# Optimization experiments

Measured on AMD Instinct MI355X. Metric: run time of the kernel, lower is better.

The kernel has to match this reference:

```python
import jax, jax.numpy as jnp
import numpy as np

NUM_EMBEDDINGS = 1024
EMBEDDING_DIM = 64
BETA = 0.25  # commitment_cost


def setup_inputs() -> dict:
    key = jax.random.key(0)
    k1, k2 = jax.random.split(key)
    z = jax.random.normal(k1, (32, EMBEDDING_DIM, 32, 32), dtype=jnp.float32)
    embedding = jax.random.normal(k2, (NUM_EMBEDDINGS, EMBEDDING_DIM), dtype=jnp.float32)
    return {"z": z, "embedding": embedding}


def reference(z, embedding):
    B, D, H, W = z.shape
    beta = jnp.asarray(BETA, z.dtype)
    # [B, D, H, W] -> [B*H*W, D]
    z_flat = jnp.transpose(z, (0, 2, 3, 1)).reshape(-1, D)
    # squared L2 distances to each code: ||z||^2 - 2 z.e^T + ||e||^2  -> [N, E]
    dist = (
        jnp.sum(z_flat * z_flat, axis=1, keepdims=True)
        - 2.0 * (z_flat @ embedding.T)
        + jnp.sum(embedding * embedding, axis=1)
    )
    encoding_indices = jnp.argmin(dist, axis=1)  # [N]
    # direct gather instead of one-hot matmul (same math)
    quantized = embedding[encoding_indices]  # [N, D]
    quantized = jnp.transpose(quantized.reshape(B, H, W, D), (0, 3, 1, 2))
    commitment_loss = beta * jnp.mean(
        (jax.lax.stop_gradient(z) - quantized) ** 2
    )
    codebook_loss = jnp.mean((z - jax.lax.stop_gradient(quantized)) ** 2)
    loss = commitment_loss + codebook_loss
    # straight-through estimator
    quantized_st = z + jax.lax.stop_gradient(quantized - z)
    return (quantized_st, loss, encoding_indices)
```

## Files before the change

kernel.cpp:

```cpp
#include <hip/hip_runtime.h>

typedef __attribute__((ext_vector_type(8))) short short8;
typedef __attribute__((ext_vector_type(4))) float f32x4;
typedef unsigned int uint32;

#define QOUT 2097152

__device__ __forceinline__ unsigned short f2bf(float f){
  uint32 u = __float_as_uint(f);
  return (unsigned short)((u + 0x7FFFu + ((u >> 16) & 1u)) >> 16);
}
__device__ __forceinline__ float bf2f(unsigned short h){
  return __uint_as_float(((uint32)h) << 16);
}
__device__ __forceinline__ uint32 med3u(uint32 a, uint32 b, uint32 c){
  uint32 d;
  asm("v_med3_u32 %0, %1, %2, %3" : "=v"(d) : "v"(a), "v"(b), "v"(c));
  return d;
}

__global__ void vq_prep(const float* __restrict__ emb, unsigned char* __restrict__ ebg,
                        float* __restrict__ nrm64, int* __restrict__ cnt){
  int u = blockIdx.x * 256 + threadIdx.x;
  if (u == 0) *cnt = 0;
  int C = u >> 3, oct = u & 7;
  const float4* e4 = reinterpret_cast<const float4*>(emb) + C * 16 + oct * 2;
  float4 v0 = e4[0], v1 = e4[1];
  float vv[8] = {v0.x, v0.y, v0.z, v0.w, v1.x, v1.y, v1.z, v1.w};
  float s = 0.f;
  short8 H, L;
#pragma unroll
  for (int j = 0; j < 8; ++j){
    float v = vv[j];
    s = fmaf(v, v, s);
    unsigned short hs = f2bf(v);
    unsigned short ls = f2bf(v - bf2f(hs));
    H[j] = (short)hs; L[j] = (short)ls;
  }
  int ng = C >> 4, c15 = C & 15, kf = oct >> 2, gg = oct & 3;
  unsigned char* base = ebg + ng * 4096 + kf * 2048 + (gg * 16 + c15) * 16;
  *reinterpret_cast<short8*>(base) = H;
  *reinterpret_cast<short8*>(base + 1024) = L;
#pragma unroll
  for (int d = 1; d < 8; d <<= 1) s += __shfl_xor(s, d);
  if (oct == 0) nrm64[C] = 0.5f * s + 128.0f;
}

__global__ __launch_bounds__(256, 2) void vq_main(
    const float* __restrict__ z, const float* __restrict__ emb,
    const unsigned char* __restrict__ ebg, const float* __restrict__ nrm64,
    float* __restrict__ out, float* __restrict__ partial, int* __restrict__ cnt)
{
  __shared__ float zf[64 * 68];
  __shared__ float nrmlds[1024];
  __shared__ uint32 mg[64][2][3];
  __shared__ uint32 cand[64][3];
  __shared__ int kidx[64];
  __shared__ int flagrow[64];
  __shared__ int nflag;
  __shared__ float werr[4];
  __shared__ float red[256];
  __shared__ int isLast;

  const int t = threadIdx.x;
  const int bi = blockIdx.x;
  const int n0 = bi * 64;
  const int b = n0 >> 10;
  const int hw0 = n0 & 1023;
  const int w = t >> 6, lane = t & 63;
  const int wm = w >> 1, wn = w & 1;
  const int l15 = lane & 15, g = lane >> 4;

#pragma unroll
  for (int i = 0; i < 4; ++i) nrmlds[i * 256 + t] = nrm64[i * 256 + t];
  if (t == 255) nflag = 0;

#pragma unroll
  for (int k = 0; k < 16; ++k){
    int li = k * 256 + t;
    int d = li >> 6, j = li & 63;
    zf[j * 68 + d] = z[((b * 64 + d) << 10) + hw0 + j];
  }
  __syncthreads();

  short8 ah[2][2], al[2][2];
#pragma unroll
  for (int mf = 0; mf < 2; ++mf)
#pragma unroll
    for (int kf = 0; kf < 2; ++kf){
      int row = wm * 32 + mf * 16 + l15;
      int base = row * 68 + kf * 32 + g * 8;
      float4 q0 = *reinterpret_cast<float4*>(&zf[base]);
      float4 q1 = *reinterpret_cast<float4*>(&zf[base + 4]);
      float vv[8] = {q0.x,q0.y,q0.z,q0.w,q1.x,q1.y,q1.z,q1.w};
#pragma unroll
      for (int j = 0; j < 8; ++j){
        float v = -vv[j];
        unsigned short hs = f2bf(v);
        unsigned short ls = f2bf(v - bf2f(hs));
        ah[mf][kf][j] = (short)hs;
        al[mf][kf][j] = (short)ls;
      }
    }

  uint32 u0[8], u1[8], u2[8];
#pragma unroll
  for (int s = 0; s < 8; ++s){ u0[s] = 0xFFFFFFFFu; u1[s] = 0xFFFFFFFFu; u2[s] = 0xFFFFFFFFu; }

  const unsigned char* pbase = ebg + (wn << 17) + (lane << 4);
  short8 fb[3][4];

#pragma unroll
  for (int s = 0; s < 2; ++s){
    const unsigned char* p = pbase + (s << 12);
    fb[s][0] = *reinterpret_cast<const short8*>(p);
    fb[s][1] = *reinterpret_cast<const short8*>(p + 1024);
    fb[s][2] = *reinterpret_cast<const short8*>(p + 2048);
    fb[s][3] = *reinterpret_cast<const short8*>(p + 3072);
  }

#pragma unroll
  for (int i = 0; i < 32; ++i){
    if (i < 30){
      const unsigned char* p = pbase + ((i + 2) << 12);
      fb[(i + 2) % 3][0] = *reinterpret_cast<const short8*>(p);
      fb[(i + 2) % 3][1] = *reinterpret_cast<const short8*>(p + 1024);
      fb[(i + 2) % 3][2] = *reinterpret_cast<const short8*>(p + 2048);
      fb[(i + 2) % 3][3] = *reinterpret_cast<const short8*>(p + 3072);
    }
    __builtin_amdgcn_sched_barrier(0);
    short8 bh0 = fb[i % 3][0];
    short8 bl0 = fb[i % 3][1];
    short8 bh1 = fb[i % 3][2];
    short8 bl1 = fb[i % 3][3];
    int code = ((wn * 32 + i) << 4) + l15;
    float nv = nrmlds[code];
    f32x4 a0 = {nv, nv, nv, nv};
    f32x4 a1 = {nv, nv, nv, nv};
    a0 = __builtin_amdgcn_mfma_f32_16x16x32_bf16(ah[0][0], bh0, a0, 0,0,0);
    a0 = __builtin_amdgcn_mfma_f32_16x16x32_bf16(ah[0][1], bh1, a0, 0,0,0);
    a0 = __builtin_amdgcn_mfma_f32_16x16x32_bf16(al[0][0], bh0, a0, 0,0,0);
    a0 = __builtin_amdgcn_mfma_f32_16x16x32_bf16(al[0][1], bh1, a0, 0,0,0);
    a0 = __builtin_amdgcn_mfma_f32_16x16x32_bf16(ah[0][0], bl0, a0, 0,0,0);
    a0 = __builtin_amdgcn_mfma_f32_16x16x32_bf16(ah[0][1], bl1, a0, 0,0,0);
    a1 = __builtin_amdgcn_mfma_f32_16x16x32_bf16(ah[1][0], bh0, a1, 0,0,0);
    a1 = __builtin_amdgcn_mfma_f32_16x16x32_bf16(ah[1][1], bh1, a1, 0,0,0);
    a1 = __builtin_amdgcn_mfma_f32_16x16x32_bf16(al[1][0], bh0, a1, 0,0,0);
    a1 = __builtin_amdgcn_mfma_f32_16x16x32_bf16(al[1][1], bh1, a1, 0,0,0);
    a1 = __builtin_amdgcn_mfma_f32_16x16x32_bf16(ah[1][0], bl0, a1, 0,0,0);
    a1 = __builtin_amdgcn_mfma_f32_16x16x32_bf16(ah[1][1], bl1, a1, 0,0,0);
    uint32 kb = (uint32)code;
#pragma unroll
    for (int r = 0; r < 4; ++r){
      uint32 k0v = (__float_as_uint(a0[r]) & 0xFFFFFC00u) | kb;
      u2[r] = med3u(k0v, u1[r], u2[r]);
      u1[r] = med3u(k0v, u0[r], u1[r]);
      u0[r] = u0[r] < k0v ? u0[r] : k0v;
      uint32 k1v = (__float_as_uint(a1[r]) & 0xFFFFFC00u) | kb;
      u2[4+r] = med3u(k1v, u1[4+r], u2[4+r]);
      u1[4+r] = med3u(k1v, u0[4+r], u1[4+r]);
      u0[4+r] = u0[4+r] < k1v ? u0[4+r] : k1v;
    }
  }

#pragma unroll
  for (int dm = 1; dm < 16; dm <<= 1){
#pragma unroll
    for (int s = 0; s < 8; ++s){
      uint32 x0 = (uint32)__shfl_xor((int)u0[s], dm);
      uint32 x1 = (uint32)__shfl_xor((int)u1[s], dm);
      uint32 x2 = (uint32)__shfl_xor((int)u2[s], dm);
      u2[s] = med3u(x0, u1[s], u2[s]); u1[s] = med3u(x0, u0[s], u1[s]); u0[s] = u0[s] < x0 ? u0[s] : x0;
      u2[s] = med3u(x1, u1[s], u2[s]); u1[s] = med3u(x1, u0[s], u1[s]); u0[s] = u0[s] < x1 ? u0[s] : x1;
      u2[s] = med3u(x2, u1[s], u2[s]); u1[s] = med3u(x2, u0[s], u1[s]); u0[s] = u0[s] < x2 ? u0[s] : x2;
    }
  }
  if (l15 == 0){
#pragma unroll
    for (int mf = 0; mf < 2; ++mf)
#pragma unroll
      for (int r = 0; r < 4; ++r){
        int lr = wm * 32 + mf * 16 + g * 4 + r;
        int s = mf * 4 + r;
        mg[lr][wn][0] = u0[s]; mg[lr][wn][1] = u1[s]; mg[lr][wn][2] = u2[s];
      }
  }
  __syncthreads();

  if (t < 64){
    uint32 a0k = mg[t][0][0], a1k = mg[t][0][1], a2k = mg[t][0][2];
#pragma unroll
    for (int j2 = 0; j2 < 3; ++j2){
      uint32 x = mg[t][1][j2];
      a2k = med3u(x, a1k, a2k); a1k = med3u(x, a0k, a1k); a0k = a0k < x ? a0k : x;
    }
    kidx[t] = (int)(a0k & 1023u);
    cand[t][0] = a0k; cand[t][1] = a1k; cand[t][2] = a2k;
    float d0 = __uint_as_float(a0k & 0xFFFFFC00u);
    float d1 = __uint_as_float(a1k & 0xFFFFFC00u);
    if (d1 - d0 < 0.0625f){
      int pos = atomicAdd(&nflag, 1);
      flagrow[pos] = t;
    }
  }
  __syncthreads();

  {
    int nf = nflag;
    int cidx = lane >> 4, q = lane & 15;
    for (int n = w; n < nf; n += 4){
      int row = flagrow[n];
      double acc = 0.0;
      if (cidx < 3){
        int k = (int)(cand[row][cidx] & 1023u);
        float4 ev = *reinterpret_cast<const float4*>(emb + k * 64 + q * 4);
        float4 zv = *reinterpret_cast<const float4*>(&zf[row * 68 + q * 4]);
        double d0v = (double)zv.x - (double)ev.x;
        double d1v = (double)zv.y - (double)ev.y;
        double d2v = (double)zv.z - (double)ev.z;
        double d3v = (double)zv.w - (double)ev.w;
        acc = d0v*d0v + d1v*d1v + d2v*d2v + d3v*d3v;
      }
#pragma unroll
      for (int dx = 1; dx < 16; dx <<= 1) acc += __shfl_xor(acc, dx);
      double s0 = __shfl(acc, 0);
      double s1 = __shfl(acc, 16);
      double s2 = __shfl(acc, 32);
      if (lane == 0){
        int k0 = (int)(cand[row][0] & 1023u);
        int k1 = (int)(cand[row][1] & 1023u);
        int k2 = (int)(cand[row][2] & 1023u);
        int bk = k0; double bs = s0;
        if (s1 < bs || (s1 == bs && k1 < bk)) { bs = s1; bk = k1; }
        if (s2 < bs || (s2 == bs && k2 < bk)) { bs = s2; bk = k2; }
        kidx[row] = bk;
      }
    }
  }
  __syncthreads();

  {
    int row = t & 63, dp = t >> 6;
    int k = kidx[row];
    const float4* e4p = reinterpret_cast<const float4*>(emb + k * 64 + dp * 16);
    float4 ev0 = e4p[0], ev1 = e4p[1], ev2 = e4p[2], ev3 = e4p[3];
    float evf[16] = {ev0.x,ev0.y,ev0.z,ev0.w, ev1.x,ev1.y,ev1.z,ev1.w,
                     ev2.x,ev2.y,ev2.z,ev2.w, ev3.x,ev3.y,ev3.z,ev3.w};
    float* ob = out + (b << 16) + hw0 + row;
    float err = 0.f;
#pragma unroll
    for (int dd = 0; dd < 16; ++dd){
      int d = dp * 16 + dd;
      float zv = zf[row * 68 + d];
      float qv = evf[dd];
      ob[d << 10] = qv;
      float df = zv - qv;
      err = fmaf(df, df, err);
    }
    if (dp == 0) out[QOUT + 1 + n0 + row] = (float)k;
#pragma unroll
    for (int dx = 1; dx < 64; dx <<= 1) err += __shfl_xor(err, dx);
    if (lane == 0) werr[w] = err;
  }
  __syncthreads();
  if (t == 0){
    partial[bi] = (werr[0] + werr[1]) + (werr[2] + werr[3]);
    __threadfence();
    int pos = atomicAdd(cnt, 1);
    isLast = (pos == 511) ? 1 : 0;
  }
  __syncthreads();

  if (isLast){
    __threadfence();
    const volatile float* vp = partial;
    red[t] = vp[t] + vp[t + 256];
    __syncthreads();
    for (int ww = 128; ww > 0; ww >>= 1){
      if (t < ww) red[t] += red[t + ww];
      __syncthreads();
    }
    if (t == 0) out[QOUT] = 1.25f * red[0] * (1.0f / 2097152.0f);
  }
}

extern "C" void kernel_launch(void* const* d_in, const int* in_sizes, int n_in,
                              void* d_out, int out_size, void* d_ws, size_t ws_size,
                              hipStream_t stream) {
  const float* z   = (const float*)d_in[0];
  const float* emb = (const float*)d_in[1];
  float* out = (float*)d_out;
  unsigned char* ebg = (unsigned char*)d_ws;
  float* nrm64   = (float*)(ebg + 262144);
  float* partial = nrm64 + 1024;
  int*   cnt     = (int*)(partial + 512);

  vq_prep <<<32,  256, 0, stream>>>(emb, ebg, nrm64, cnt);
  vq_main <<<512, 256, 0, stream>>>(z, emb, ebg, nrm64, out, partial, cnt);
}
```

Baseline: 43.46 us.

## Split codebook scan across eight waves per block and drop manual prefetch

```diff
diff --git a/kernel.cpp b/kernel.cpp
--- a/kernel.cpp
+++ b/kernel.cpp
@@ -46,19 +46,19 @@
   if (oct == 0) nrm64[C] = 0.5f * s + 128.0f;
 }
 
-__global__ __launch_bounds__(256, 2) void vq_main(
+__global__ __launch_bounds__(512, 4) void vq_main(
     const float* __restrict__ z, const float* __restrict__ emb,
     const unsigned char* __restrict__ ebg, const float* __restrict__ nrm64,
     float* __restrict__ out, float* __restrict__ partial, int* __restrict__ cnt)
 {
   __shared__ float zf[64 * 68];
   __shared__ float nrmlds[1024];
-  __shared__ uint32 mg[64][2][3];
+  __shared__ uint32 mg[64][4][3];
   __shared__ uint32 cand[64][3];
   __shared__ int kidx[64];
   __shared__ int flagrow[64];
   __shared__ int nflag;
-  __shared__ float werr[4];
+  __shared__ float werr[8];
   __shared__ float red[256];
   __shared__ int isLast;
 
@@ -68,16 +68,16 @@
   const int b = n0 >> 10;
   const int hw0 = n0 & 1023;
   const int w = t >> 6, lane = t & 63;
-  const int wm = w >> 1, wn = w & 1;
+  const int wm = w >> 2, wn = w & 3;
   const int l15 = lane & 15, g = lane >> 4;
 
 #pragma unroll
-  for (int i = 0; i < 4; ++i) nrmlds[i * 256 + t] = nrm64[i * 256 + t];
-  if (t == 255) nflag = 0;
-
-#pragma unroll
-  for (int k = 0; k < 16; ++k){
-    int li = k * 256 + t;
+  for (int i = 0; i < 2; ++i) nrmlds[i * 512 + t] = nrm64[i * 512 + t];
+  if (t == 0) nflag = 0;
+
+#pragma unroll
+  for (int k = 0; k < 8; ++k){
+    int li = k * 512 + t;
     int d = li >> 6, j = li & 63;
     zf[j * 68 + d] = z[((b * 64 + d) << 10) + hw0 + j];
   }
@@ -107,33 +107,15 @@
 #pragma unroll
   for (int s = 0; s < 8; ++s){ u0[s] = 0xFFFFFFFFu; u1[s] = 0xFFFFFFFFu; u2[s] = 0xFFFFFFFFu; }
 
-  const unsigned char* pbase = ebg + (wn << 17) + (lane << 4);
-  short8 fb[3][4];
-
-#pragma unroll
-  for (int s = 0; s < 2; ++s){
-    const unsigned char* p = pbase + (s << 12);
-    fb[s][0] = *reinterpret_cast<const short8*>(p);
-    fb[s][1] = *reinterpret_cast<const short8*>(p + 1024);
-    fb[s][2] = *reinterpret_cast<const short8*>(p + 2048);
-    fb[s][3] = *reinterpret_cast<const short8*>(p + 3072);
-  }
-
-#pragma unroll
-  for (int i = 0; i < 32; ++i){
-    if (i < 30){
-      const unsigned char* p = pbase + ((i + 2) << 12);
-      fb[(i + 2) % 3][0] = *reinterpret_cast<const short8*>(p);
-      fb[(i + 2) % 3][1] = *reinterpret_cast<const short8*>(p + 1024);
-      fb[(i + 2) % 3][2] = *reinterpret_cast<const short8*>(p + 2048);
-      fb[(i + 2) % 3][3] = *reinterpret_cast<const short8*>(p + 3072);
-    }
-    __builtin_amdgcn_sched_barrier(0);
-    short8 bh0 = fb[i % 3][0];
-    short8 bl0 = fb[i % 3][1];
-    short8 bh1 = fb[i % 3][2];
-    short8 bl1 = fb[i % 3][3];
-    int code = ((wn * 32 + i) << 4) + l15;
+  const unsigned char* pbase = ebg + (wn << 16) + (lane << 4);
+#pragma unroll
+  for (int i = 0; i < 16; ++i){
+    const unsigned char* p = pbase + (i << 12);
+    short8 bh0 = *reinterpret_cast<const short8*>(p);
+    short8 bl0 = *reinterpret_cast<const short8*>(p + 1024);
+    short8 bh1 = *reinterpret_cast<const short8*>(p + 2048);
+    short8 bl1 = *reinterpret_cast<const short8*>(p + 3072);
+    int code = ((wn * 16 + i) << 4) + l15;
     float nv = nrmlds[code];
     f32x4 a0 = {nv, nv, nv, nv};
     f32x4 a1 = {nv, nv, nv, nv};
@@ -190,10 +172,12 @@
   if (t < 64){
     uint32 a0k = mg[t][0][0], a1k = mg[t][0][1], a2k = mg[t][0][2];
 #pragma unroll
-    for (int j2 = 0; j2 < 3; ++j2){
-      uint32 x = mg[t][1][j2];
-      a2k = med3u(x, a1k, a2k); a1k = med3u(x, a0k, a1k); a0k = a0k < x ? a0k : x;
-    }
+    for (int v = 1; v < 4; ++v)
+#pragma unroll
+      for (int j2 = 0; j2 < 3; ++j2){
+        uint32 x = mg[t][v][j2];
+        a2k = med3u(x, a1k, a2k); a1k = med3u(x, a0k, a1k); a0k = a0k < x ? a0k : x;
+      }
     kidx[t] = (int)(a0k & 1023u);
     cand[t][0] = a0k; cand[t][1] = a1k; cand[t][2] = a2k;
     float d0 = __uint_as_float(a0k & 0xFFFFFC00u);
@@ -208,7 +192,7 @@
   {
     int nf = nflag;
     int cidx = lane >> 4, q = lane & 15;
-    for (int n = w; n < nf; n += 4){
+    for (int n = w; n < nf; n += 8){
       int row = flagrow[n];
       double acc = 0.0;
       if (cidx < 3){
@@ -242,15 +226,14 @@
   {
     int row = t & 63, dp = t >> 6;
     int k = kidx[row];
-    const float4* e4p = reinterpret_cast<const float4*>(emb + k * 64 + dp * 16);
-    float4 ev0 = e4p[0], ev1 = e4p[1], ev2 = e4p[2], ev3 = e4p[3];
-    float evf[16] = {ev0.x,ev0.y,ev0.z,ev0.w, ev1.x,ev1.y,ev1.z,ev1.w,
-                     ev2.x,ev2.y,ev2.z,ev2.w, ev3.x,ev3.y,ev3.z,ev3.w};
+    const float4* e4p = reinterpret_cast<const float4*>(emb + k * 64 + dp * 8);
+    float4 ev0 = e4p[0], ev1 = e4p[1];
+    float evf[8] = {ev0.x,ev0.y,ev0.z,ev0.w, ev1.x,ev1.y,ev1.z,ev1.w};
     float* ob = out + (b << 16) + hw0 + row;
     float err = 0.f;
 #pragma unroll
-    for (int dd = 0; dd < 16; ++dd){
-      int d = dp * 16 + dd;
+    for (int dd = 0; dd < 8; ++dd){
+      int d = dp * 8 + dd;
       float zv = zf[row * 68 + d];
       float qv = evf[dd];
       ob[d << 10] = qv;
@@ -264,7 +247,8 @@
   }
   __syncthreads();
   if (t == 0){
-    partial[bi] = (werr[0] + werr[1]) + (werr[2] + werr[3]);
+    partial[bi] = ((werr[0] + werr[1]) + (werr[2] + werr[3]))
+                + ((werr[4] + werr[5]) + (werr[6] + werr[7]));
     __threadfence();
     int pos = atomicAdd(cnt, 1);
     isLast = (pos == 511) ? 1 : 0;
@@ -273,8 +257,10 @@
 
   if (isLast){
     __threadfence();
-    const volatile float* vp = partial;
-    red[t] = vp[t] + vp[t + 256];
+    if (t < 256){
+      const volatile float* vp = partial;
+      red[t] = vp[t] + vp[t + 256];
+    }
     __syncthreads();
     for (int ww = 128; ww > 0; ww >>= 1){
       if (t < ww) red[t] += red[t + ww];
@@ -296,5 +282,5 @@
   int*   cnt     = (int*)(partial + 512);
 
   vq_prep <<<32,  256, 0, stream>>>(emb, ebg, nrm64, cnt);
-  vq_main <<<512, 256, 0, stream>>>(z, emb, ebg, nrm64, out, partial, cnt);
-}
+  vq_main <<<512, 512, 0, stream>>>(z, emb, ebg, nrm64, out, partial, cnt);
+}
```

New measurement: 45.70 us. +5.2%, slower.

## Stage codebook chunks in LDS via global_load_lds with swizzled layout

Applied to the files above, without the earlier changes.

```diff
diff --git a/kernel.cpp b/kernel.cpp
--- a/kernel.cpp
+++ b/kernel.cpp
@@ -17,6 +17,11 @@
   uint32 d;
   asm("v_med3_u32 %0, %1, %2, %3" : "=v"(d) : "v"(a), "v"(b), "v"(c));
   return d;
+}
+__device__ __forceinline__ void glds16(const unsigned char* g, unsigned char* l){
+  __builtin_amdgcn_global_load_lds(
+      (const __attribute__((address_space(1))) unsigned int*)g,
+      (__attribute__((address_space(3))) unsigned int*)l, 16, 0, 0);
 }
 
 __global__ void vq_prep(const float* __restrict__ emb, unsigned char* __restrict__ ebg,
@@ -24,23 +29,25 @@
   int u = blockIdx.x * 256 + threadIdx.x;
   if (u == 0) *cnt = 0;
   int C = u >> 3, oct = u & 7;
-  const float4* e4 = reinterpret_cast<const float4*>(emb) + C * 16 + oct * 2;
-  float4 v0 = e4[0], v1 = e4[1];
-  float vv[8] = {v0.x, v0.y, v0.z, v0.w, v1.x, v1.y, v1.z, v1.w};
+  int chunk = C >> 8, cc = C & 255;
+  unsigned char* eb = ebg + chunk * 65536;
+  int x = (cc & 7) << 1;
+  const float4* e4 = reinterpret_cast<const float4*>(emb) + C * 16;
   float s = 0.f;
-  short8 H, L;
-#pragma unroll
-  for (int j = 0; j < 8; ++j){
-    float v = vv[j];
-    s = fmaf(v, v, s);
-    unsigned short hs = f2bf(v);
-    unsigned short ls = f2bf(v - bf2f(hs));
-    H[j] = (short)hs; L[j] = (short)ls;
-  }
-  int ng = C >> 4, c15 = C & 15, kf = oct >> 2, gg = oct & 3;
-  unsigned char* base = ebg + ng * 4096 + kf * 2048 + (gg * 16 + c15) * 16;
-  *reinterpret_cast<short8*>(base) = H;
-  *reinterpret_cast<short8*>(base + 1024) = L;
+#pragma unroll
+  for (int si = 0; si < 2; ++si){
+    int sub = oct * 2 + si;
+    float4 v = e4[sub];
+    s += v.x*v.x + v.y*v.y + v.z*v.z + v.w*v.w;
+    ushort4 h, l;
+    h.x = f2bf(v.x); l.x = f2bf(v.x - bf2f(h.x));
+    h.y = f2bf(v.y); l.y = f2bf(v.y - bf2f(h.y));
+    h.z = f2bf(v.z); l.z = f2bf(v.z - bf2f(h.z));
+    h.w = f2bf(v.w); l.w = f2bf(v.w - bf2f(h.w));
+    int off = cc * 128 + ((sub ^ x) << 3);
+    *reinterpret_cast<ushort4*>(eb + off) = h;
+    *reinterpret_cast<ushort4*>(eb + 32768 + off) = l;
+  }
 #pragma unroll
   for (int d = 1; d < 8; d <<= 1) s += __shfl_xor(s, d);
   if (oct == 0) nrm64[C] = 0.5f * s + 128.0f;
@@ -51,7 +58,7 @@
     const unsigned char* __restrict__ ebg, const float* __restrict__ nrm64,
     float* __restrict__ out, float* __restrict__ partial, int* __restrict__ cnt)
 {
-  __shared__ float zf[64 * 68];
+  __shared__ __align__(16) unsigned char LB[65536];
   __shared__ float nrmlds[1024];
   __shared__ uint32 mg[64][2][3];
   __shared__ uint32 cand[64][3];
@@ -71,10 +78,10 @@
   const int wm = w >> 1, wn = w & 1;
   const int l15 = lane & 15, g = lane >> 4;
 
-#pragma unroll
-  for (int i = 0; i < 4; ++i) nrmlds[i * 256 + t] = nrm64[i * 256 + t];
-  if (t == 255) nflag = 0;
-
+  for (int i = t; i < 1024; i += 256) nrmlds[i] = nrm64[i];
+  if (t == 0) nflag = 0;
+
+  float* zf = reinterpret_cast<float*>(LB);
 #pragma unroll
   for (int k = 0; k < 16; ++k){
     int li = k * 256 + t;
@@ -102,65 +109,63 @@
         al[mf][kf][j] = (short)ls;
       }
     }
+  __syncthreads();
 
   uint32 u0[8], u1[8], u2[8];
 #pragma unroll
   for (int s = 0; s < 8; ++s){ u0[s] = 0xFFFFFFFFu; u1[s] = 0xFFFFFFFFu; u2[s] = 0xFFFFFFFFu; }
 
-  const unsigned char* pbase = ebg + (wn << 17) + (lane << 4);
-  short8 fb[3][4];
-
-#pragma unroll
-  for (int s = 0; s < 2; ++s){
-    const unsigned char* p = pbase + (s << 12);
-    fb[s][0] = *reinterpret_cast<const short8*>(p);
-    fb[s][1] = *reinterpret_cast<const short8*>(p + 1024);
-    fb[s][2] = *reinterpret_cast<const short8*>(p + 2048);
-    fb[s][3] = *reinterpret_cast<const short8*>(p + 3072);
-  }
-
-#pragma unroll
-  for (int i = 0; i < 32; ++i){
-    if (i < 30){
-      const unsigned char* p = pbase + ((i + 2) << 12);
-      fb[(i + 2) % 3][0] = *reinterpret_cast<const short8*>(p);
-      fb[(i + 2) % 3][1] = *reinterpret_cast<const short8*>(p + 1024);
-      fb[(i + 2) % 3][2] = *reinterpret_cast<const short8*>(p + 2048);
-      fb[(i + 2) % 3][3] = *reinterpret_cast<const short8*>(p + 3072);
-    }
-    __builtin_amdgcn_sched_barrier(0);
-    short8 bh0 = fb[i % 3][0];
-    short8 bl0 = fb[i % 3][1];
-    short8 bh1 = fb[i % 3][2];
-    short8 bl1 = fb[i % 3][3];
-    int code = ((wn * 32 + i) << 4) + l15;
-    float nv = nrmlds[code];
-    f32x4 a0 = {nv, nv, nv, nv};
-    f32x4 a1 = {nv, nv, nv, nv};
-    a0 = __builtin_amdgcn_mfma_f32_16x16x32_bf16(ah[0][0], bh0, a0, 0,0,0);
-    a0 = __builtin_amdgcn_mfma_f32_16x16x32_bf16(ah[0][1], bh1, a0, 0,0,0);
-    a0 = __builtin_amdgcn_mfma_f32_16x16x32_bf16(al[0][0], bh0, a0, 0,0,0);
-    a0 = __builtin_amdgcn_mfma_f32_16x16x32_bf16(al[0][1], bh1, a0, 0,0,0);
-    a0 = __builtin_amdgcn_mfma_f32_16x16x32_bf16(ah[0][0], bl0, a0, 0,0,0);
-    a0 = __builtin_amdgcn_mfma_f32_16x16x32_bf16(ah[0][1], bl1, a0, 0,0,0);
-    a1 = __builtin_amdgcn_mfma_f32_16x16x32_bf16(ah[1][0], bh0, a1, 0,0,0);
-    a1 = __builtin_amdgcn_mfma_f32_16x16x32_bf16(ah[1][1], bh1, a1, 0,0,0);
-    a1 = __builtin_amdgcn_mfma_f32_16x16x32_bf16(al[1][0], bh0, a1, 0,0,0);
-    a1 = __builtin_amdgcn_mfma_f32_16x16x32_bf16(al[1][1], bh1, a1, 0,0,0);
-    a1 = __builtin_amdgcn_mfma_f32_16x16x32_bf16(ah[1][0], bl0, a1, 0,0,0);
-    a1 = __builtin_amdgcn_mfma_f32_16x16x32_bf16(ah[1][1], bl1, a1, 0,0,0);
-    uint32 kb = (uint32)code;
-#pragma unroll
-    for (int r = 0; r < 4; ++r){
-      uint32 k0v = (__float_as_uint(a0[r]) & 0xFFFFFC00u) | kb;
-      u2[r] = med3u(k0v, u1[r], u2[r]);
-      u1[r] = med3u(k0v, u0[r], u1[r]);
-      u0[r] = u0[r] < k0v ? u0[r] : k0v;
-      uint32 k1v = (__float_as_uint(a1[r]) & 0xFFFFFC00u) | kb;
-      u2[4+r] = med3u(k1v, u1[4+r], u2[4+r]);
-      u1[4+r] = med3u(k1v, u0[4+r], u1[4+r]);
-      u0[4+r] = u0[4+r] < k1v ? u0[4+r] : k1v;
-    }
+  const int cc0 = wn * 128 + l15;
+  const int xsw = (l15 & 7) << 1;
+  const int v0s = ((g * 2) ^ xsw) << 3;
+  const int v1s = ((8 + g * 2) ^ xsw) << 3;
+
+  for (int c = 0; c < 4; ++c){
+    const unsigned char* src = ebg + c * 65536;
+#pragma unroll
+    for (int r = 0; r < 16; ++r){
+      int off = (r * 4 + w) * 1024;
+      glds16(src + off + lane * 16, LB + off);
+    }
+    __syncthreads();
+
+#pragma unroll
+    for (int nf = 0; nf < 8; ++nf){
+      int cc = cc0 + nf * 16;
+      const unsigned char* rb = LB + cc * 128;
+      short8 bh0 = *reinterpret_cast<const short8*>(rb + v0s);
+      short8 bh1 = *reinterpret_cast<const short8*>(rb + v1s);
+      short8 bl0 = *reinterpret_cast<const short8*>(rb + 32768 + v0s);
+      short8 bl1 = *reinterpret_cast<const short8*>(rb + 32768 + v1s);
+      float nv = nrmlds[(c << 8) + cc];
+      f32x4 a0 = {nv, nv, nv, nv};
+      f32x4 a1 = {nv, nv, nv, nv};
+      a0 = __builtin_amdgcn_mfma_f32_16x16x32_bf16(ah[0][0], bh0, a0, 0,0,0);
+      a0 = __builtin_amdgcn_mfma_f32_16x16x32_bf16(ah[0][1], bh1, a0, 0,0,0);
+      a0 = __builtin_amdgcn_mfma_f32_16x16x32_bf16(al[0][0], bh0, a0, 0,0,0);
+      a0 = __builtin_amdgcn_mfma_f32_16x16x32_bf16(al[0][1], bh1, a0, 0,0,0);
+      a0 = __builtin_amdgcn_mfma_f32_16x16x32_bf16(ah[0][0], bl0, a0, 0,0,0);
+      a0 = __builtin_amdgcn_mfma_f32_16x16x32_bf16(ah[0][1], bl1, a0, 0,0,0);
+      a1 = __builtin_amdgcn_mfma_f32_16x16x32_bf16(ah[1][0], bh0, a1, 0,0,0);
+      a1 = __builtin_amdgcn_mfma_f32_16x16x32_bf16(ah[1][1], bh1, a1, 0,0,0);
+      a1 = __builtin_amdgcn_mfma_f32_16x16x32_bf16(al[1][0], bh0, a1, 0,0,0);
+      a1 = __builtin_amdgcn_mfma_f32_16x16x32_bf16(al[1][1], bh1, a1, 0,0,0);
+      a1 = __builtin_amdgcn_mfma_f32_16x16x32_bf16(ah[1][0], bl0, a1, 0,0,0);
+      a1 = __builtin_amdgcn_mfma_f32_16x16x32_bf16(ah[1][1], bl1, a1, 0,0,0);
+      uint32 kb = (uint32)((c << 8) | cc0 | (nf << 4));
+#pragma unroll
+      for (int r = 0; r < 4; ++r){
+        uint32 k0v = (__float_as_uint(a0[r]) & 0xFFFFFC00u) | kb;
+        u2[r] = med3u(k0v, u1[r], u2[r]);
+        u1[r] = med3u(k0v, u0[r], u1[r]);
+        u0[r] = u0[r] < k0v ? u0[r] : k0v;
+        uint32 k1v = (__float_as_uint(a1[r]) & 0xFFFFFC00u) | kb;
+        u2[4+r] = med3u(k1v, u1[4+r], u2[4+r]);
+        u1[4+r] = med3u(k1v, u0[4+r], u1[4+r]);
+        u0[4+r] = u0[4+r] < k1v ? u0[4+r] : k1v;
+      }
+    }
+    __syncthreads();
   }
 
 #pragma unroll
@@ -207,18 +212,18 @@
 
   {
     int nf = nflag;
-    int cidx = lane >> 4, q = lane & 15;
+    int cidx = lane >> 4, qd = lane & 15;
     for (int n = w; n < nf; n += 4){
       int row = flagrow[n];
       double acc = 0.0;
       if (cidx < 3){
         int k = (int)(cand[row][cidx] & 1023u);
-        float4 ev = *reinterpret_cast<const float4*>(emb + k * 64 + q * 4);
-        float4 zv = *reinterpret_cast<const float4*>(&zf[row * 68 + q * 4]);
-        double d0v = (double)zv.x - (double)ev.x;
-        double d1v = (double)zv.y - (double)ev.y;
-        double d2v = (double)zv.z - (double)ev.z;
-        double d3v = (double)zv.w - (double)ev.w;
+        const float* zrow = z + (b << 16) + hw0 + row;
+        float4 ev = *reinterpret_cast<const float4*>(emb + k * 64 + qd * 4);
+        double d0v = (double)zrow[(qd * 4 + 0) << 10] - (double)ev.x;
+        double d1v = (double)zrow[(qd * 4 + 1) << 10] - (double)ev.y;
+        double d2v = (double)zrow[(qd * 4 + 2) << 10] - (double)ev.z;
+        double d3v = (double)zrow[(qd * 4 + 3) << 10] - (double)ev.w;
         acc = d0v*d0v + d1v*d1v + d2v*d2v + d3v*d3v;
       }
 #pragma unroll
@@ -246,12 +251,13 @@
     float4 ev0 = e4p[0], ev1 = e4p[1], ev2 = e4p[2], ev3 = e4p[3];
     float evf[16] = {ev0.x,ev0.y,ev0.z,ev0.w, ev1.x,ev1.y,ev1.z,ev1.w,
                      ev2.x,ev2.y,ev2.z,ev2.w, ev3.x,ev3.y,ev3.z,ev3.w};
+    const float* zb = z + (b << 16) + hw0 + row;
     float* ob = out + (b << 16) + hw0 + row;
     float err = 0.f;
 #pragma unroll
     for (int dd = 0; dd < 16; ++dd){
       int d = dp * 16 + dd;
-      float zv = zf[row * 68 + d];
+      float zv = zb[d << 10];
       float qv = evf[dd];
       ob[d << 10] = qv;
       float df = zv - qv;
```

Measured after the change: 46.98 us. 1.08x slower.
